# Performance work log

Hardware: AMD Instinct MI355X
Metric: run time of the kernel (lower is better)

The kernel has to match this reference:

```python
import jax, jax.numpy as jnp
import numpy as np

EMB = 1024
HEADS = 16
HD = EMB // HEADS
EPS = 1e-5

def _ln(x, g, b):
    m = jnp.mean(x, axis=-1, keepdims=True)
    v = jnp.mean((x - m) ** 2, axis=-1, keepdims=True)
    return (x - m) * jax.lax.rsqrt(v + EPS) * g + b

def setup_inputs() -> dict:
    key = jax.random.key(0)
    ks = jax.random.split(key, 12)
    s_in = 1.0 / np.sqrt(EMB)
    s_ff = 1.0 / np.sqrt(4 * EMB)
    return {
        "x": jax.random.normal(ks[0], (2, 2048, EMB), jnp.float32),
        "wq": jax.random.uniform(ks[1], (HEADS, EMB, HD), jnp.float32, -s_in, s_in),
        "wk": jax.random.uniform(ks[2], (HEADS, EMB, HD), jnp.float32, -s_in, s_in),
        "wv": jax.random.uniform(ks[3], (HEADS, EMB, HD), jnp.float32, -s_in, s_in),
        "wo": jax.random.uniform(ks[4], (EMB, EMB), jnp.float32, -s_in, s_in),
        "bo": jax.random.uniform(ks[5], (EMB,), jnp.float32, -s_in, s_in),
        "g1": jnp.ones((EMB,), jnp.float32),
        "b1": jnp.zeros((EMB,), jnp.float32),
        "g2": jnp.ones((EMB,), jnp.float32),
        "b2": jnp.zeros((EMB,), jnp.float32),
        "w1": jax.random.uniform(ks[6], (EMB, 4 * EMB), jnp.float32, -s_in, s_in),
        "bf1": jax.random.uniform(ks[7], (4 * EMB,), jnp.float32, -s_in, s_in),
        "w2": jax.random.uniform(ks[8], (4 * EMB, EMB), jnp.float32, -s_ff, s_ff),
        "bf2": jax.random.uniform(ks[9], (EMB,), jnp.float32, -s_ff, s_ff),
    }

def reference(x, wq, wk, wv, wo, bo, g1, b1, g2, b2, w1, bf1, w2, bf2):
    B, T, C = x.shape
    h = _ln(x, g1, b1)
    # all heads batched: [B,H,T,HD]
    q = jnp.einsum('btc,hcd->bhtd', h, wq)
    k = jnp.einsum('btc,hcd->bhtd', h, wk)
    v = jnp.einsum('btc,hcd->bhtd', h, wv)
    # NOTE: original scales by full emb_size C**-0.5, not head_size
    scores = jnp.einsum('bhtd,bhsd->bhts', q, k) * (C ** -0.5)
    causal = jnp.tril(jnp.ones((T, T), bool))
    scores = jnp.where(causal, scores, -jnp.inf)
    w = jax.nn.softmax(scores, axis=-1)
    attn = jnp.einsum('bhts,bhsd->bhtd', w, v)
    attn = attn.transpose(0, 2, 1, 3).reshape(B, T, C)  # concat heads
    x = x + attn @ wo + bo
    h2 = _ln(x, g2, b2)
    ffn = jax.nn.relu(h2 @ w1 + bf1) @ w2 + bf2
    return x + ffn
```

## Files before the change

kernel.cpp:

```cpp
#include <hip/hip_runtime.h>
#include <hip/hip_bf16.h>

typedef __bf16 bf16x8 __attribute__((ext_vector_type(8)));
typedef float f32x4 __attribute__((ext_vector_type(4)));
typedef short s16x8 __attribute__((ext_vector_type(8)));

#define DEV __device__ __forceinline__

DEV float b2f(unsigned short u) {
  unsigned int x = ((unsigned int)u) << 16;
  return __builtin_bit_cast(float, x);
}
DEV unsigned short f2b(float f) {
  unsigned int x = __builtin_bit_cast(unsigned int, f);
  x += 0x7fffu + ((x >> 16) & 1u);
  return (unsigned short)(x >> 16);
}
DEV unsigned int f2b2(float a, float b) {
  float2 t; t.x = a; t.y = b;
  __hip_bfloat162 v = __float22bfloat162_rn(t);
  unsigned int r;
  __builtin_memcpy(&r, &v, 4);
  return r;
}
DEV f32x4 mfma16(bf16x8 a, bf16x8 b, f32x4 c) {
  return __builtin_amdgcn_mfma_f32_16x16x32_bf16(a, b, c, 0, 0, 0);
}
DEV void gl2lds16(const unsigned short* g, unsigned short* l) {
  __builtin_amdgcn_global_load_lds(
      (const __attribute__((address_space(1))) void*)g,
      (__attribute__((address_space(3))) void*)l, 16, 0, 0);
}

__global__ __launch_bounds__(256)
void transpose_k(const float* __restrict__ in, unsigned short* __restrict__ out,
                 int K, int N, long zin, long zout) {
  __shared__ float tile[32][33];
  in  += (size_t)blockIdx.z * zin;
  out += (size_t)blockIdx.z * zout;
  int n0 = blockIdx.x * 32, k0 = blockIdx.y * 32;
  int tx = threadIdx.x, ty = threadIdx.y;
  #pragma unroll
  for (int i = ty; i < 32; i += 8)
    tile[i][tx] = in[(size_t)(k0 + i) * N + n0 + tx];
  __syncthreads();
  #pragma unroll
  for (int i = ty; i < 32; i += 8)
    out[(size_t)(n0 + i) * K + k0 + tx] = f2b(tile[tx][i]);
}

__global__ __launch_bounds__(256)
void transpose_qkv(const float* __restrict__ wq, const float* __restrict__ wk,
                   const float* __restrict__ wv, unsigned short* __restrict__ out) {
  __shared__ float tile[32][33];
  const int z = blockIdx.z;
  const float* in = (z < 16) ? (wq + (size_t)z * 65536)
                  : (z < 32) ? (wk + (size_t)(z - 16) * 65536)
                             : (wv + (size_t)(z - 32) * 65536);
  unsigned short* o = out + (size_t)z * 65536;
  int n0 = blockIdx.x * 32, k0 = blockIdx.y * 32;
  int tx = threadIdx.x, ty = threadIdx.y;
  #pragma unroll
  for (int i = ty; i < 32; i += 8)
    tile[i][tx] = in[(size_t)(k0 + i) * 64 + n0 + tx];
  __syncthreads();
  #pragma unroll
  for (int i = ty; i < 32; i += 8)
    o[(size_t)(n0 + i) * 1024 + k0 + tx] = f2b(tile[tx][i]);
}

__global__ __launch_bounds__(256)
void ln_kernel(const float* __restrict__ x, const float* __restrict__ g,
               const float* __restrict__ b, unsigned short* __restrict__ o) {
  __shared__ float rs[4];
  __shared__ float rq[4];
  int row = blockIdx.x, tid = threadIdx.x;
  const float* xr = x + (size_t)row * 1024;
  float4 raw = ((const float4*)xr)[tid];
  float s = raw.x + raw.y + raw.z + raw.w;
  float q = raw.x*raw.x + raw.y*raw.y + raw.z*raw.z + raw.w*raw.w;
  #pragma unroll
  for (int off = 32; off > 0; off >>= 1) {
    s += __shfl_down(s, off);
    q += __shfl_down(q, off);
  }
  int wave = tid >> 6;
  if ((tid & 63) == 0) { rs[wave] = s; rq[wave] = q; }
  __syncthreads();
  float ts = rs[0] + rs[1] + rs[2] + rs[3];
  float tq = rq[0] + rq[1] + rq[2] + rq[3];
  float mean = ts * (1.0f/1024.0f);
  float var = tq * (1.0f/1024.0f) - mean*mean;
  float rstd = rsqrtf(var + 1e-5f);
  float4 gr = ((const float4*)g)[tid];
  float4 br = ((const float4*)b)[tid];
  float o0 = (raw.x-mean)*rstd*gr.x + br.x;
  float o1 = (raw.y-mean)*rstd*gr.y + br.y;
  float o2 = (raw.z-mean)*rstd*gr.z + br.z;
  float o3 = (raw.w-mean)*rstd*gr.w + br.w;
  uint2 ov;
  ov.x = f2b2(o0, o1);
  ov.y = f2b2(o2, o3);
  ((uint2*)(o + (size_t)row * 1024))[tid] = ov;
}

template<bool RELU, bool BIAS, bool VFUSE>
__global__ __launch_bounds__(512, 2)
void gemm8p(const unsigned short* __restrict__ A, const unsigned short* __restrict__ Bt,
            const float* __restrict__ bias, void* __restrict__ Cv,
            unsigned short* __restrict__ vT, int NTn, int N, int K) {
  __shared__ unsigned short As[4][256*32];
  __shared__ unsigned short Bs[4][256*32];
  const int tid = threadIdx.x;
  const int lane = tid & 63, wave = tid >> 6;
  const int quad = lane >> 4, l16 = lane & 15;
  const int wm = wave >> 2, wn = wave & 3;
  const int nwg = gridDim.x;
  const int id = blockIdx.x;
  const int id2 = (id & 7) * (nwg >> 3) + (id >> 3);
  const int mt = id2 / NTn, nt = id2 % NTn;
  const int m0 = mt * 256, n0 = nt * 256;

  f32x4 acc[8][4];
  #pragma unroll
  for (int i = 0; i < 8; ++i)
    #pragma unroll
    for (int j = 0; j < 4; ++j) acc[i][j] = (f32x4){0.f, 0.f, 0.f, 0.f};

  const int srow = tid >> 2;
  const int scc  = (((tid & 3) ^ ((srow >> 1) & 3)) * 8);
  const unsigned short* Ab = A + (size_t)m0 * K;
  const unsigned short* Bb = Bt + (size_t)n0 * K;

  const int NT = K >> 5;
  const int H  = NT << 2;

  auto stage = [&](int h) {
    const int Tt = h >> 2, part = h & 3, kk = Tt << 5;
    const int buf = Tt & 3;
    if (part == 0)
      gl2lds16(Ab + (size_t)srow * K + kk + scc,         &As[buf][tid * 8]);
    else if (part == 1)
      gl2lds16(Ab + (size_t)(srow + 128) * K + kk + scc, &As[buf][4096 + tid * 8]);
    else if (part == 2)
      gl2lds16(Bb + (size_t)srow * K + kk + scc,         &Bs[buf][tid * 8]);
    else
      gl2lds16(Bb + (size_t)(srow + 128) * K + kk + scc, &Bs[buf][4096 + tid * 8]);
  };

  #pragma unroll
  for (int h = 0; h < 10; ++h) stage(h);
  asm volatile("s_waitcnt vmcnt(6)" ::: "memory");
  asm volatile("s_barrier" ::: "memory");

  const int qsw = (quad ^ ((l16 >> 1) & 3)) * 8;
  const int arow0 = wm * 128 + l16;
  const int brow0 = wn * 64 + l16;

  for (int T = 0; T < NT; ++T) {
    const int buf = T & 3;
    bf16x8 bq[4];
    {
      bf16x8 af[4];
      #pragma unroll
      for (int i = 0; i < 4; ++i)
        af[i] = __builtin_bit_cast(bf16x8,
          *(const s16x8*)&As[buf][(arow0 + i*16)*32 + qsw]);
      #pragma unroll
      for (int j = 0; j < 4; ++j)
        bq[j] = __builtin_bit_cast(bf16x8,
          *(const s16x8*)&Bs[buf][(brow0 + j*16)*32 + qsw]);
      const int h = 4*T + 10;
      if (h < H)     stage(h);
      if (h + 1 < H) stage(h + 1);
      asm volatile("s_barrier" ::: "memory");
      __builtin_amdgcn_s_setprio(1);
      #pragma unroll
      for (int i = 0; i < 4; ++i)
        #pragma unroll
        for (int j = 0; j < 4; ++j)
          acc[i][j] = mfma16(af[i], bq[j], acc[i][j]);
      __builtin_amdgcn_s_setprio(0);
      asm volatile("s_barrier" ::: "memory");
    }
    {
      bf16x8 af[4];
      #pragma unroll
      for (int i = 0; i < 4; ++i)
        af[i] = __builtin_bit_cast(bf16x8,
          *(const s16x8*)&As[buf][(arow0 + 64 + i*16)*32 + qsw]);
      const int h = 4*T + 12;
      if (h < H)     stage(h);
      if (h + 1 < H) stage(h + 1);
      if (T + 3 < NT)      { asm volatile("s_waitcnt vmcnt(6)" ::: "memory"); }
      else if (T + 2 < NT) { asm volatile("s_waitcnt vmcnt(4)" ::: "memory"); }
      else if (T + 1 < NT) { asm volatile("s_waitcnt vmcnt(0)" ::: "memory"); }
      asm volatile("s_barrier" ::: "memory");
      __builtin_amdgcn_s_setprio(1);
      #pragma unroll
      for (int i = 0; i < 4; ++i)
        #pragma unroll
        for (int j = 0; j < 4; ++j)
          acc[4 + i][j] = mfma16(af[i], bq[j], acc[4 + i][j]);
      __builtin_amdgcn_s_setprio(0);
      asm volatile("s_barrier" ::: "memory");
    }
  }

  #pragma unroll
  for (int ii = 0; ii < 8; ++ii) {
    const int row = m0 + wm*128 + ii*16 + quad*4;
    #pragma unroll
    for (int j = 0; j < 4; ++j) {
      const int col = n0 + wn*64 + j*16 + l16;
      if (VFUSE && col >= 2048) {
        const int b = row >> 11, tloc = row & 2047;
        const int h = (col - 2048) >> 6, d = col & 63;
        ushort4 pk;
        pk.x = f2b(acc[ii][j][0]);
        pk.y = f2b(acc[ii][j][1]);
        pk.z = f2b(acc[ii][j][2]);
        pk.w = f2b(acc[ii][j][3]);
        *(ushort4*)&vT[((size_t)((b*16 + h)*64 + d))*2048 + tloc] = pk;
      } else {
        float bv = BIAS ? bias[col] : 0.f;
        #pragma unroll
        for (int r = 0; r < 4; ++r) {
          float v = acc[ii][j][r] + bv;
          if (RELU) v = fmaxf(v, 0.f);
          ((unsigned short*)Cv)[(size_t)(row + r) * N + col] = f2b(v);
        }
      }
    }
  }
}

__global__ __launch_bounds__(512)
void gemm_t128(const unsigned short* __restrict__ A, const unsigned short* __restrict__ Bt,
               const float* __restrict__ bias, const float* __restrict__ resid,
               float* __restrict__ C, int M, int N, int K) {
  __shared__ unsigned short SMEM[6*128*64];
  const int tid = threadIdx.x;
  const int lane = tid & 63;
  const int quad = lane >> 4, l16 = lane & 15;
  const int wave = tid >> 6;
  const int sub = wave >> 2;
  const int wq = wave & 3;
  const int wm = (wq >> 1) * 64, wn = (wq & 1) * 64;
  const int id = blockIdx.x;
  const int xcd = id & 7, i2 = id >> 3;
  const int mt = (xcd << 2) | (i2 >> 3);
  const int nt = i2 & 7;
  const int m0 = mt * 128, n0 = nt * 128;

  f32x4 acc[4][4];
  #pragma unroll
  for (int i = 0; i < 4; ++i)
    #pragma unroll
    for (int j = 0; j < 4; ++j) acc[i][j] = (f32x4){0.f, 0.f, 0.f, 0.f};

  const int srow = tid >> 3;
  const int scc  = ((tid & 7) ^ (srow & 7)) * 8;
  const unsigned short* Ab = A + (size_t)m0 * K;
  const unsigned short* Bb = Bt + (size_t)n0 * K;

  auto stage = [&](int buf, int k0) {
    unsigned short* Ad = SMEM + buf * 8192;
    unsigned short* Bd = SMEM + 24576 + buf * 8192;
    gl2lds16(Ab + (size_t)srow * K + k0 + scc,        Ad + tid * 8);
    gl2lds16(Ab + (size_t)(srow + 64) * K + k0 + scc, Ad + 4096 + tid * 8);
    gl2lds16(Bb + (size_t)srow * K + k0 + scc,        Bd + tid * 8);
    gl2lds16(Bb + (size_t)(srow + 64) * K + k0 + scc, Bd + 4096 + tid * 8);
  };

  const int niter = K >> 6;
  stage(0, 0);
  stage(1, 64);

  const int cc = sub * 4 + quad;
  int bufc = 0;
  for (int it = 0; it < niter; ++it) {
    if (it + 1 < niter) {
      asm volatile("s_waitcnt vmcnt(4)" ::: "memory");
    } else {
      asm volatile("s_waitcnt vmcnt(0)" ::: "memory");
    }
    __builtin_amdgcn_s_barrier();
    if (it + 2 < niter) {
      int bufn = bufc + 2; if (bufn >= 3) bufn -= 3;
      stage(bufn, (it + 2) * 64);
    }
    const unsigned short* Ar = SMEM + bufc * 8192;
    const unsigned short* Br = SMEM + 24576 + bufc * 8192;
    bf16x8 af[4], bfr[4];
    #pragma unroll
    for (int i = 0; i < 4; ++i) {
      const int R = wm + i*16 + l16;
      af[i] = __builtin_bit_cast(bf16x8,
        *(const s16x8*)&Ar[R*64 + ((cc ^ (R & 7)) * 8)]);
    }
    #pragma unroll
    for (int j = 0; j < 4; ++j) {
      const int R = wn + j*16 + l16;
      bfr[j] = __builtin_bit_cast(bf16x8,
        *(const s16x8*)&Br[R*64 + ((cc ^ (R & 7)) * 8)]);
    }
    #pragma unroll
    for (int i = 0; i < 4; ++i)
      #pragma unroll
      for (int j = 0; j < 4; ++j)
        acc[i][j] = mfma16(af[i], bfr[j], acc[i][j]);
    bufc = (bufc == 2) ? 0 : bufc + 1;
  }

  __syncthreads();
  float* ex = (float*)&SMEM[0];
  float* w = ex + wq * 4096;
  if (sub == 1) {
    #pragma unroll
    for (int i = 0; i < 4; ++i)
      #pragma unroll
      for (int j = 0; j < 4; ++j)
        *(f32x4*)&w[(i*4 + j)*256 + lane*4] = acc[i][j];
  }
  __syncthreads();
  if (sub == 1) return;

  #pragma unroll
  for (int i = 0; i < 4; ++i) {
    const int row = m0 + wm + i*16 + quad*4;
    #pragma unroll
    for (int j = 0; j < 4; ++j) {
      f32x4 oth = *(const f32x4*)&w[(i*4 + j)*256 + lane*4];
      const int col = n0 + wn + j*16 + l16;
      const float bv = bias[col];
      #pragma unroll
      for (int r = 0; r < 4; ++r)
        C[(size_t)(row + r) * N + col] =
            acc[i][j][r] + oth[r] + bv + resid[(size_t)(row + r) * N + col];
    }
  }
}

__global__ __launch_bounds__(256)
void attn_kernel(const unsigned short* __restrict__ qkv,
                 const unsigned short* __restrict__ vT,
                 unsigned short* __restrict__ outc) {
  __shared__ unsigned short Ks[2][64*64];
  __shared__ unsigned short Vs[2][64*64];
  __shared__ unsigned short Ps[2][4*16*64];
  const int tid = threadIdx.x, lane = tid & 63, wave = tid >> 6;
  const int quad = lane >> 4, l16 = lane & 15;
  const int id = blockIdx.x;
  const int xcd = id & 7;
  const int bh = xcd * 4 + ((id >> 3) & 3);
  const int jA = id >> 5, jB = 31 - jA;
  const int b = bh >> 4, h = bh & 15;
  const size_t tokbase = (size_t)b * 2048 * 3072;
  const unsigned short* Q  = qkv + tokbase + h * 64;
  const unsigned short* Kg = qkv + tokbase + 1024 + h * 64;
  const unsigned short* Vg = vT + (size_t)bh * 64 * 2048;

  const s16x8 ones_s = {0x3F80, 0x3F80, 0x3F80, 0x3F80, 0x3F80, 0x3F80, 0x3F80, 0x3F80};
  const bf16x8 onesf = __builtin_bit_cast(bf16x8, ones_s);

  bf16x8 qf[2][2];
  #pragma unroll
  for (int t = 0; t < 2; ++t) {
    const int qrow = (t ? jB : jA) * 64 + wave * 16 + l16;
    #pragma unroll
    for (int s = 0; s < 2; ++s) {
      s16x8 raw = *(const s16x8*)(Q + (size_t)qrow * 3072 + s * 32 + quad * 8);
      unsigned short* rp = (unsigned short*)&raw;
      #pragma unroll
      for (int k = 0; k < 8; ++k) rp[k] = f2b(b2f(rp[k]) * 0.0450842305f);
      qf[t][s] = __builtin_bit_cast(bf16x8, raw);
    }
  }

  f32x4 accO[2][4];
  f32x4 accS[2] = {(f32x4){0.f,0.f,0.f,0.f}, (f32x4){0.f,0.f,0.f,0.f}};
  #pragma unroll
  for (int t = 0; t < 2; ++t)
    #pragma unroll
    for (int i = 0; i < 4; ++i) accO[t][i] = (f32x4){0.f, 0.f, 0.f, 0.f};

  const int r8 = lane >> 3;
  const int cs = (((lane & 7) ^ r8) * 8);

  auto stage = [&](int buf, int kv0) {
    #pragma unroll
    for (int i = 0; i < 2; ++i) {
      int row = wave * 16 + i * 8;
      gl2lds16(Kg + (size_t)(kv0 + row + r8) * 3072 + cs, &Ks[buf][row * 64 + lane * 8]);
      gl2lds16(Vg + (size_t)(row + r8) * 2048 + kv0 + cs, &Vs[buf][row * 64 + lane * 8]);
    }
  };

  const int prow = (wave*16 + l16) * 64;
  const int pq7  = l16 & 7;

  const int ntile = jB + 1;
  stage(0, 0);
  __syncthreads();

  for (int it = 0; it < ntile; ++it) {
    const int buf = it & 1;
    if (it + 1 < ntile) stage(buf ^ 1, (it + 1) * 64);
    const bool act0 = (it <= jA);

    #pragma unroll
    for (int t = 0; t < 2; ++t) {
      if (t == 0 && !act0) continue;
      const int jT = t ? jB : jA;
      f32x4 sv[4];
      #pragma unroll
      for (int ni = 0; ni < 4; ++ni) {
        sv[ni] = (f32x4){0.f, 0.f, 0.f, 0.f};
        #pragma unroll
        for (int s = 0; s < 2; ++s) {
          bf16x8 kf = __builtin_bit_cast(bf16x8,
            *(const s16x8*)&Ks[buf][(ni*16 + l16)*64 + (((s*4 + quad) ^ (l16 & 7)) * 8)]);
          sv[ni] = mfma16(kf, qf[t][s], sv[ni]);
        }
      }
      if (it == jT) {
        const int qr = jT*64 + wave*16 + l16;
        const int kvb = it*64 + quad*4;
        #pragma unroll
        for (int ni = 0; ni < 4; ++ni) {
          #pragma unroll
          for (int r = 0; r < 4; ++r)
            if (kvb + ni*16 + r > qr) sv[ni][r] = -__builtin_inff();
        }
      }
      #pragma unroll
      for (int ni = 0; ni < 4; ++ni) {
        float p0 = exp2f(sv[ni][0]);
        float p1 = exp2f(sv[ni][1]);
        float p2 = exp2f(sv[ni][2]);
        float p3 = exp2f(sv[ni][3]);
        uint2 pk2;
        pk2.x = f2b2(p0, p1);
        pk2.y = f2b2(p2, p3);
        const int pc = ((2*ni + (quad >> 1)) ^ pq7) * 8 + (quad & 1) * 4;
        *(uint2*)&Ps[t][prow + pc] = pk2;
      }
    }
    __asm__ volatile("s_waitcnt lgkmcnt(0)" ::: "memory");

    #pragma unroll
    for (int t = 0; t < 2; ++t) {
      if (t == 0 && !act0) continue;
      #pragma unroll
      for (int s = 0; s < 2; ++s) {
        bf16x8 pf = __builtin_bit_cast(bf16x8,
          *(const s16x8*)&Ps[t][prow + (((s*4 + quad) ^ pq7) * 8)]);
        accS[t] = mfma16(pf, onesf, accS[t]);
        #pragma unroll
        for (int ni = 0; ni < 4; ++ni) {
          bf16x8 vf = __builtin_bit_cast(bf16x8,
            *(const s16x8*)&Vs[buf][(ni*16 + l16)*64 + (((s*4 + quad) ^ (l16 & 7)) * 8)]);
          accO[t][ni] = mfma16(pf, vf, accO[t][ni]);
        }
      }
    }
    __syncthreads();
  }

  #pragma unroll
  for (int t = 0; t < 2; ++t) {
    const int rowg = (t ? jB : jA)*64 + wave*16 + quad*4;
    float inv[4];
    #pragma unroll
    for (int r = 0; r < 4; ++r) inv[r] = __builtin_amdgcn_rcpf(accS[t][r]);
    #pragma unroll
    for (int ni = 0; ni < 4; ++ni)
      #pragma unroll
      for (int r = 0; r < 4; ++r)
        outc[(size_t)(b*2048 + rowg + r) * 1024 + h*64 + ni*16 + l16]
          = f2b(accO[t][ni][r] * inv[r]);
  }
}

extern "C" void kernel_launch(void* const* d_in, const int* in_sizes, int n_in,
                              void* d_out, int out_size, void* d_ws, size_t ws_size,
                              hipStream_t stream) {
  (void)in_sizes; (void)n_in; (void)out_size; (void)ws_size;
  const float* x   = (const float*)d_in[0];
  const float* wq  = (const float*)d_in[1];
  const float* wk  = (const float*)d_in[2];
  const float* wv  = (const float*)d_in[3];
  const float* wo  = (const float*)d_in[4];
  const float* bo  = (const float*)d_in[5];
  const float* g1  = (const float*)d_in[6];
  const float* b1  = (const float*)d_in[7];
  const float* g2  = (const float*)d_in[8];
  const float* b2  = (const float*)d_in[9];
  const float* w1  = (const float*)d_in[10];
  const float* bf1 = (const float*)d_in[11];
  const float* w2  = (const float*)d_in[12];
  const float* bf2 = (const float*)d_in[13];
  float* out = (float*)d_out;

  unsigned short* ws    = (unsigned short*)d_ws;
  unsigned short* wqkvt = ws;
  unsigned short* wot   = wqkvt + 3*1024*1024;
  unsigned short* w1t   = wot   + 1024*1024;
  unsigned short* w2t   = w1t   + 4096*1024;
  unsigned short* hbuf  = w2t   + 4096*1024;
  unsigned short* qkvb  = hbuf  + 4096*1024;
  unsigned short* attnb = qkvb  + (size_t)4096*3072;
  float*          x2b   = (float*)(attnb + 4096*1024);
  unsigned short* vTb   = (unsigned short*)x2b;
  unsigned short* midb  = qkvb;

  dim3 tb(32, 8);
  transpose_qkv<<<dim3(2,32,48), tb, 0, stream>>>(wq, wk, wv, wqkvt);
  transpose_k<<<dim3(32,32,1),  tb, 0, stream>>>(wo, wot, 1024, 1024, 0, 0);
  transpose_k<<<dim3(128,32,1), tb, 0, stream>>>(w1, w1t, 1024, 4096, 0, 0);
  transpose_k<<<dim3(32,128,1), tb, 0, stream>>>(w2, w2t, 4096, 1024, 0, 0);

  ln_kernel<<<4096, 256, 0, stream>>>(x, g1, b1, hbuf);
  gemm8p<false,false,true><<<192, 512, 0, stream>>>(
      hbuf, wqkvt, nullptr, qkvb, vTb, 12, 3072, 1024);
  attn_kernel<<<512, 256, 0, stream>>>(qkvb, vTb, attnb);
  gemm_t128<<<256, 512, 0, stream>>>(attnb, wot, bo, x, x2b, 4096, 1024, 1024);
  ln_kernel<<<4096, 256, 0, stream>>>(x2b, g2, b2, hbuf);
  gemm8p<true,true,false><<<256, 512, 0, stream>>>(
      hbuf, w1t, bf1, midb, nullptr, 16, 4096, 1024);
  gemm_t128<<<256, 512, 0, stream>>>(midb, w2t, bf2, x2b, out, 4096, 1024, 4096);
}
```

Baseline: 321.5 us.

## Triple-buffer K/V tiles with explicit vmcnt waits and share fragment loads across query tiles

The attention kernel moves from double- to triple-buffered K/V LDS staging, prefetching two tiles ahead. It replaces __syncthreads with raw s_barrier plus vmcnt-counted waits, so only the oldest tile's loads have to complete. It also reads each K and V fragment once and uses it for both query tiles, which halves LDS reads for those operands but computes scores for the inactive tile too. The cost is extra LDS, which may lower occupancy, and some wasted MFMA work on inactive tiles.

Result: no change. 326.4 us (+1.5%).

```diff
diff --git a/kernel.cpp b/kernel.cpp
--- a/kernel.cpp
+++ b/kernel.cpp
@@ -346,8 +346,8 @@
 void attn_kernel(const unsigned short* __restrict__ qkv,
                  const unsigned short* __restrict__ vT,
                  unsigned short* __restrict__ outc) {
-  __shared__ unsigned short Ks[2][64*64];
-  __shared__ unsigned short Vs[2][64*64];
+  __shared__ unsigned short Ks[3][64*64];
+  __shared__ unsigned short Vs[3][64*64];
   __shared__ unsigned short Ps[2][4*16*64];
   const int tid = threadIdx.x, lane = tid & 63, wave = tid >> 6;
   const int quad = lane >> 4, l16 = lane & 15;
@@ -402,44 +402,61 @@
 
   const int ntile = jB + 1;
   stage(0, 0);
-  __syncthreads();
-
+  stage(1, 64);
+  asm volatile("s_waitcnt vmcnt(4)" ::: "memory");
+  __builtin_amdgcn_s_barrier();
+
+  int bufc = 0;
   for (int it = 0; it < ntile; ++it) {
-    const int buf = it & 1;
-    if (it + 1 < ntile) stage(buf ^ 1, (it + 1) * 64);
+    if (it + 2 < ntile) {
+      int bufn = bufc + 2; if (bufn >= 3) bufn -= 3;
+      stage(bufn, (it + 2) * 64);
+    }
     const bool act0 = (it <= jA);
-
+    const unsigned short* Kb = &Ks[bufc][0];
+    const unsigned short* Vb = &Vs[bufc][0];
+
+    f32x4 sv[2][4];
+    #pragma unroll
+    for (int t = 0; t < 2; ++t)
+      #pragma unroll
+      for (int ni = 0; ni < 4; ++ni) sv[t][ni] = (f32x4){0.f, 0.f, 0.f, 0.f};
+    #pragma unroll
+    for (int s = 0; s < 2; ++s)
+      #pragma unroll
+      for (int ni = 0; ni < 4; ++ni) {
+        bf16x8 kf = __builtin_bit_cast(bf16x8,
+          *(const s16x8*)&Kb[(ni*16 + l16)*64 + (((s*4 + quad) ^ (l16 & 7)) * 8)]);
+        sv[0][ni] = mfma16(kf, qf[0][s], sv[0][ni]);
+        sv[1][ni] = mfma16(kf, qf[1][s], sv[1][ni]);
+      }
+    if (it == jA) {
+      const int qr = jA*64 + wave*16 + l16;
+      const int kvb = it*64 + quad*4;
+      #pragma unroll
+      for (int ni = 0; ni < 4; ++ni)
+        #pragma unroll
+        for (int r = 0; r < 4; ++r)
+          if (kvb + ni*16 + r > qr) sv[0][ni][r] = -__builtin_inff();
+    }
+    if (it == jB) {
+      const int qr = jB*64 + wave*16 + l16;
+      const int kvb = it*64 + quad*4;
+      #pragma unroll
+      for (int ni = 0; ni < 4; ++ni)
+        #pragma unroll
+        for (int r = 0; r < 4; ++r)
+          if (kvb + ni*16 + r > qr) sv[1][ni][r] = -__builtin_inff();
+    }
     #pragma unroll
     for (int t = 0; t < 2; ++t) {
       if (t == 0 && !act0) continue;
-      const int jT = t ? jB : jA;
-      f32x4 sv[4];
       #pragma unroll
       for (int ni = 0; ni < 4; ++ni) {
-        sv[ni] = (f32x4){0.f, 0.f, 0.f, 0.f};
-        #pragma unroll
-        for (int s = 0; s < 2; ++s) {
-          bf16x8 kf = __builtin_bit_cast(bf16x8,
-            *(const s16x8*)&Ks[buf][(ni*16 + l16)*64 + (((s*4 + quad) ^ (l16 & 7)) * 8)]);
-          sv[ni] = mfma16(kf, qf[t][s], sv[ni]);
-        }
-      }
-      if (it == jT) {
-        const int qr = jT*64 + wave*16 + l16;
-        const int kvb = it*64 + quad*4;
-        #pragma unroll
-        for (int ni = 0; ni < 4; ++ni) {
-          #pragma unroll
-          for (int r = 0; r < 4; ++r)
-            if (kvb + ni*16 + r > qr) sv[ni][r] = -__builtin_inff();
-        }
-      }
-      #pragma unroll
-      for (int ni = 0; ni < 4; ++ni) {
-        float p0 = exp2f(sv[ni][0]);
-        float p1 = exp2f(sv[ni][1]);
-        float p2 = exp2f(sv[ni][2]);
-        float p3 = exp2f(sv[ni][3]);
+        float p0 = exp2f(sv[t][ni][0]);
+        float p1 = exp2f(sv[t][ni][1]);
+        float p2 = exp2f(sv[t][ni][2]);
+        float p3 = exp2f(sv[t][ni][3]);
         uint2 pk2;
         pk2.x = f2b2(p0, p1);
         pk2.y = f2b2(p2, p3);
@@ -450,22 +467,32 @@
     __asm__ volatile("s_waitcnt lgkmcnt(0)" ::: "memory");
 
     #pragma unroll
-    for (int t = 0; t < 2; ++t) {
-      if (t == 0 && !act0) continue;
-      #pragma unroll
-      for (int s = 0; s < 2; ++s) {
-        bf16x8 pf = __builtin_bit_cast(bf16x8,
-          *(const s16x8*)&Ps[t][prow + (((s*4 + quad) ^ pq7) * 8)]);
-        accS[t] = mfma16(pf, onesf, accS[t]);
-        #pragma unroll
-        for (int ni = 0; ni < 4; ++ni) {
-          bf16x8 vf = __builtin_bit_cast(bf16x8,
-            *(const s16x8*)&Vs[buf][(ni*16 + l16)*64 + (((s*4 + quad) ^ (l16 & 7)) * 8)]);
-          accO[t][ni] = mfma16(pf, vf, accO[t][ni]);
-        }
+    for (int s = 0; s < 2; ++s) {
+      bf16x8 pf1 = __builtin_bit_cast(bf16x8,
+        *(const s16x8*)&Ps[1][prow + (((s*4 + quad) ^ pq7) * 8)]);
+      accS[1] = mfma16(pf1, onesf, accS[1]);
+      bf16x8 pf0;
+      if (act0) {
+        pf0 = __builtin_bit_cast(bf16x8,
+          *(const s16x8*)&Ps[0][prow + (((s*4 + quad) ^ pq7) * 8)]);
+        accS[0] = mfma16(pf0, onesf, accS[0]);
       }
-    }
-    __syncthreads();
+      #pragma unroll
+      for (int ni = 0; ni < 4; ++ni) {
+        bf16x8 vf = __builtin_bit_cast(bf16x8,
+          *(const s16x8*)&Vb[(ni*16 + l16)*64 + (((s*4 + quad) ^ (l16 & 7)) * 8)]);
+        accO[1][ni] = mfma16(pf1, vf, accO[1][ni]);
+        if (act0) accO[0][ni] = mfma16(pf0, vf, accO[0][ni]);
+      }
+    }
+
+    if (it + 2 < ntile) {
+      asm volatile("s_waitcnt vmcnt(4)" ::: "memory");
+    } else if (it + 1 < ntile) {
+      asm volatile("s_waitcnt vmcnt(0)" ::: "memory");
+    }
+    __builtin_amdgcn_s_barrier();
+    bufc = (bufc == 2) ? 0 : bufc + 1;
   }
 
   #pragma unroll
```
